# Optimization experiments

Measured on AMD Instinct MI355X. Metric: run time of the kernel, lower is better.

## Reference

```python
import jax, jax.numpy as jnp
import numpy as np

B, C1, C2 = 8, 256, 256
Cc = 128          # c = int(c2 * e)
RED = 16          # reduction in FrequencyModulation
HEADS = 8
HD = Cc // HEADS  # 16
HH, WW = 32, 32


def _c1x1(x, w, b=None):
    # 1x1 conv as channel contraction; w: [out_c, in_c]
    y = jnp.einsum('bchw,oc->bohw', x, w)
    return y if b is None else y + b[None, :, None, None]


def setup_inputs() -> dict:
    key = jax.random.key(0)
    ks = jax.random.split(key, 22)
    s = 0.02
    p = {}
    p['x'] = jax.random.normal(ks[0], (B, C1, HH, WW), jnp.float32)
    p['cv1_w'] = jax.random.normal(ks[1], (2 * Cc, C1), jnp.float32) * s
    p['cv1_b'] = jnp.zeros((2 * Cc,), jnp.float32)
    # FrequencyModulation params
    p['fm_w1'] = jax.random.normal(ks[2], (Cc // RED, Cc), jnp.float32) * s
    p['fm_w2'] = jax.random.normal(ks[3], (Cc, Cc // RED), jnp.float32) * s
    p['ca_w1'] = jax.random.normal(ks[4], (Cc // RED, Cc), jnp.float32) * s
    p['ca_w2'] = jax.random.normal(ks[5], (Cc, Cc // RED), jnp.float32) * s
    # TokenStatisticsSelfAttention params (qkv_bias=False)
    p['qkv_w'] = jax.random.normal(ks[6], (3 * Cc, Cc), jnp.float32) * s
    p['tproj_w'] = jax.random.normal(ks[7], (Cc, Cc), jnp.float32) * s
    p['tproj_b'] = jnp.zeros((Cc,), jnp.float32)
    # SpatialQuantizedRouter params
    p['dw_w'] = jax.random.normal(ks[8], (Cc, 1, 3, 3), jnp.float32) * s  # depthwise
    p['dw_b'] = jnp.zeros((Cc,), jnp.float32)
    p['rt_w'] = jax.random.normal(ks[9], (1, Cc), jnp.float32) * s
    p['rt_b'] = jnp.zeros((1,), jnp.float32)
    p['q_w'] = jax.random.normal(ks[10], (Cc, Cc), jnp.float32) * s
    p['k_w'] = jax.random.normal(ks[11], (Cc, Cc), jnp.float32) * s
    p['v_w'] = jax.random.normal(ks[12], (Cc, Cc), jnp.float32) * s
    p['sproj_w'] = jax.random.normal(ks[13], (Cc, Cc), jnp.float32) * s
    p['sproj_b'] = jnp.zeros((Cc,), jnp.float32)
    p['cv2_w'] = jax.random.normal(ks[14], (C2, 3 * Cc), jnp.float32) * s
    p['cv2_b'] = jnp.zeros((C2,), jnp.float32)
    return p


def _forward(x, cv1_w, cv1_b, fm_w1, fm_w2, ca_w1, ca_w2, qkv_w, tproj_w,
             tproj_b, dw_w, dw_b, rt_w, rt_b, q_w, k_w, v_w, sproj_w,
             sproj_b, cv2_w, cv2_b):
    Bb, _, H, W = x.shape
    N = H * W
    y = _c1x1(x, cv1_w, cv1_b)
    y0, y1 = y[:, :Cc], y[:, Cc:]

    # ---- Branch 1: FrequencyModulation ----
    xf = jnp.fft.rfft2(y1.astype(jnp.float32), norm='ortho')  # [B,c,H,W//2+1] complex
    mag = jnp.abs(xf)
    pooled = mag.mean(axis=(-2, -1))                          # [B,c]
    fw = jax.nn.sigmoid(jax.nn.relu(pooled @ fm_w1.T) @ fm_w2.T)  # [B,c]
    # mag*fw*exp(i*phase) == fw * xf  (fw is real, per batch/channel)
    xs = jnp.fft.irfft2(xf * fw[:, :, None, None].astype(jnp.complex64),
                        s=(H, W), norm='ortho')               # [B,c,H,W]
    ca = jax.nn.sigmoid(jax.nn.relu(xs.mean(axis=(-2, -1)) @ ca_w1.T) @ ca_w2.T)
    freq_out = xs * ca[:, :, None, None]

    # ---- Branch 2: TokenStatisticsSelfAttention ----
    xt = y1.reshape(Bb, Cc, N).transpose(0, 2, 1)             # [B,N,c]
    qkv = (xt @ qkv_w.T).reshape(Bb, N, 3, HEADS, HD).transpose(2, 0, 3, 1, 4)
    q, k, v = qkv[0], qkv[1], qkv[2]                          # [B,h,N,d]
    var_v = jnp.var(v, axis=-1, ddof=1, keepdims=True)        # [B,h,N,1] (unbiased)
    var_k = jnp.var(k, axis=-1, ddof=1, keepdims=True)
    attn = jax.nn.softmax(jnp.einsum('bhnx,bhmx->bhnm', var_v, var_k) * (HD ** -0.5), axis=-1)
    to = jnp.einsum('bhnm,bhmd->bhnd', attn, v).transpose(0, 2, 1, 3).reshape(Bb, N, Cc)
    stat_out = ((to @ tproj_w.T) + tproj_b).transpose(0, 2, 1).reshape(Bb, Cc, H, W)

    # ---- Branch 3: SpatialQuantizedRouter (training-mode blend) ----
    x_local = jax.lax.conv_general_dilated(
        y1, dw_w, (1, 1), 'SAME', feature_group_count=Cc,
        dimension_numbers=('NCHW', 'OIHW', 'NCHW')) + dw_b[None, :, None, None]
    p_route = jax.nn.sigmoid(y1.mean(axis=(-2, -1)) @ rt_w.T + rt_b)  # [B,1]
    qb = jnp.sign(_c1x1(y1, q_w).reshape(Bb, Cc, N))
    kb = jnp.sign(_c1x1(y1, k_w).reshape(Bb, Cc, N))
    vv = _c1x1(y1, v_w).reshape(Bb, Cc, N)
    a2 = jax.nn.softmax(jnp.einsum('bcn,bcm->bnm', qb, kb) * (Cc ** -0.5), axis=-1)
    # torch: bmm(v, attn.T) -> out[b,c,n] = sum_m v[b,c,m]*attn[b,n,m]
    ob = jnp.einsum('bcm,bnm->bcn', vv, a2).reshape(Bb, Cc, H, W)
    out_bin = _c1x1(ob, sproj_w, sproj_b)
    alpha = p_route.reshape(Bb, 1, 1, 1)
    spat_out = (1.0 - alpha) * x_local + alpha * out_bin

    attn_out = freq_out + stat_out + spat_out
    yc = jnp.concatenate([y0, y1, attn_out], axis=1)          # [B,3c,H,W]
    out = _c1x1(yc, cv2_w, cv2_b)
    return x + out  # add: shortcut and c1 == c2


def reference(x, cv1_w, cv1_b, fm_w1, fm_w2, ca_w1, ca_w2, qkv_w, tproj_w,
              tproj_b, dw_w, dw_b, rt_w, rt_b, q_w, k_w, v_w, sproj_w,
              sproj_b, cv2_w, cv2_b):
    return _forward(x, cv1_w, cv1_b, fm_w1, fm_w2, ca_w1, ca_w2, qkv_w,
                    tproj_w, tproj_b, dw_w, dw_b, rt_w, rt_b, q_w, k_w, v_w,
                    sproj_w, sproj_b, cv2_w, cv2_b)
```

## Files before the change

### kernel.cpp

```cpp
#include <hip/hip_runtime.h>
#include <math.h>

#define BATCH 8
#define NPIX 1024

typedef __attribute__((ext_vector_type(8))) short short8v;
typedef __attribute__((ext_vector_type(4))) float f32x4;

__device__ inline unsigned short f2bf(float x) {
  unsigned int u = __float_as_uint(x);
  return (unsigned short)((u + 0x7FFFu + ((u >> 16) & 1u)) >> 16);
}
__device__ inline float bf2f(unsigned short h) {
  return __uint_as_float((unsigned int)h << 16);
}
__device__ inline unsigned long long pack4bf(float a, float b, float c, float d) {
  return (unsigned long long)(unsigned short)f2bf(a) |
         ((unsigned long long)(unsigned short)f2bf(b) << 16) |
         ((unsigned long long)(unsigned short)f2bf(c) << 32) |
         ((unsigned long long)(unsigned short)f2bf(d) << 48);
}

__global__ __launch_bounds__(256) void convw_kernel(
    const float* __restrict__ cv1_w, const float* __restrict__ qkv_w,
    const float* __restrict__ tproj_w, const float* __restrict__ sproj_w,
    const float* __restrict__ cv2_w, const float* __restrict__ q_w,
    const float* __restrict__ k_w, const float* __restrict__ v_w,
    short* __restrict__ wb) {
  int i = blockIdx.x * 256 + threadIdx.x;
  float v;
  if (i < 65536) v = cv1_w[i];
  else if (i < 163840) {
    int j = i - 65536;
    if (j < 49152) v = qkv_w[j];
    else {
      int jj = j - 49152, wsel = jj >> 14, r = jj & 16383;
      v = (wsel == 0) ? q_w[r] : (wsel == 1) ? k_w[r] : v_w[r];
    }
  }
  else if (i < 180224) v = tproj_w[i - 163840];
  else if (i < 196608) v = sproj_w[i - 180224];
  else v = cv2_w[i - 196608];
  wb[i] = (short)f2bf(v);
}

template<int MODE, bool HAS_BIAS, bool HAS_RES, bool XF32T, bool EMIT_HI>
__global__ __launch_bounds__(256) void mgemm_kernel(
    const short* __restrict__ Wb, const void* __restrict__ Xsrc, int ldx,
    const float* __restrict__ bias, const float* __restrict__ res,
    void* __restrict__ Y0, void* __restrict__ Y1,
    int K, long sXT, long sY, long sR, int tStride, int tOff) {
  __shared__ __align__(16) short As[64][40];
  __shared__ __align__(16) short Bs[64][40];
  const int b = blockIdx.z;
  const int n0 = blockIdx.x * 64, m0 = blockIdx.y * 64;
  const int tid = threadIdx.x;
  const int l = tid & 63, w = tid >> 6;
  const int wm = w >> 1, wn = w & 1;
  const int sr = tid >> 2, sko = (tid & 3) * 8;
  const int xr = tid >> 3, xcg = (tid & 7) * 8;
  const int fr = l & 15, fk = (l >> 4) * 8;
  f32x4 acc[2][2] = {};
  for (int k0 = 0; k0 < K; k0 += 32) {
    *(uint4*)&As[sr][sko] = *(const uint4*)(Wb + (long)(m0 + sr) * K + k0 + sko);
    if (XF32T) {
      const float* Xf = (const float*)Xsrc + (long)b * sXT;
      const float4 xa = *(const float4*)(Xf + (long)(k0 + xr) * 1024 + n0 + xcg);
      const float4 xb = *(const float4*)(Xf + (long)(k0 + xr) * 1024 + n0 + xcg + 4);
      Bs[xcg + 0][xr] = (short)f2bf(xa.x); Bs[xcg + 1][xr] = (short)f2bf(xa.y);
      Bs[xcg + 2][xr] = (short)f2bf(xa.z); Bs[xcg + 3][xr] = (short)f2bf(xa.w);
      Bs[xcg + 4][xr] = (short)f2bf(xb.x); Bs[xcg + 5][xr] = (short)f2bf(xb.y);
      Bs[xcg + 6][xr] = (short)f2bf(xb.z); Bs[xcg + 7][xr] = (short)f2bf(xb.w);
    } else {
      const short* Xb = (const short*)Xsrc + (long)b * sXT;
      *(uint4*)&Bs[sr][sko] = *(const uint4*)(Xb + (long)(n0 + sr) * ldx + k0 + sko);
    }
    __syncthreads();
    short8v a0 = *(short8v*)&As[wm * 32 + fr][fk];
    short8v a1 = *(short8v*)&As[wm * 32 + 16 + fr][fk];
    short8v b0 = *(short8v*)&Bs[wn * 32 + fr][fk];
    short8v b1 = *(short8v*)&Bs[wn * 32 + 16 + fr][fk];
    acc[0][0] = __builtin_amdgcn_mfma_f32_16x16x32_bf16(a0, b0, acc[0][0], 0, 0, 0);
    acc[0][1] = __builtin_amdgcn_mfma_f32_16x16x32_bf16(a0, b1, acc[0][1], 0, 0, 0);
    acc[1][0] = __builtin_amdgcn_mfma_f32_16x16x32_bf16(a1, b0, acc[1][0], 0, 0, 0);
    acc[1][1] = __builtin_amdgcn_mfma_f32_16x16x32_bf16(a1, b1, acc[1][1], 0, 0, 0);
    __syncthreads();
  }
#pragma unroll
  for (int tm = 0; tm < 2; tm++) {
    const int m_base = m0 + wm * 32 + tm * 16 + (l >> 4) * 4;
#pragma unroll
    for (int tn = 0; tn < 2; tn++) {
      const int n = n0 + wn * 32 + tn * 16 + (l & 15);
      float v0 = acc[tm][tn][0], v1 = acc[tm][tn][1];
      float v2 = acc[tm][tn][2], v3 = acc[tm][tn][3];
      if (HAS_BIAS) {
        v0 += bias[m_base]; v1 += bias[m_base + 1];
        v2 += bias[m_base + 2]; v3 += bias[m_base + 3];
      }
      if (HAS_RES) {
        v0 += res[(long)b * sR + (long)(m_base + 0) * 1024 + n];
        v1 += res[(long)b * sR + (long)(m_base + 1) * 1024 + n];
        v2 += res[(long)b * sR + (long)(m_base + 2) * 1024 + n];
        v3 += res[(long)b * sR + (long)(m_base + 3) * 1024 + n];
      }
      if (MODE == 0) {
        float* Y = (float*)Y0 + (long)b * sY + n;
        Y[(long)(m_base + 0) * 1024] = v0; Y[(long)(m_base + 1) * 1024] = v1;
        Y[(long)(m_base + 2) * 1024] = v2; Y[(long)(m_base + 3) * 1024] = v3;
      } else if (MODE == 1) {
        short* Y = (short*)Y0 + (long)b * sY + n;
        Y[(long)(m_base + 0) * 1024] = (short)f2bf(v0);
        Y[(long)(m_base + 1) * 1024] = (short)f2bf(v1);
        Y[(long)(m_base + 2) * 1024] = (short)f2bf(v2);
        Y[(long)(m_base + 3) * 1024] = (short)f2bf(v3);
      } else if (MODE == 2) {
        *(unsigned long long*)((short*)Y0 + ((long)b * 1024 + n) * tStride +
                               tOff + m_base) = pack4bf(v0, v1, v2, v3);
        if (EMIT_HI && m_base >= 128) {
          float* Y = (float*)Y1 + ((long)b * 128 + m_base - 128) * 1024 + n;
          Y[0] = v0; Y[1024] = v1; Y[2048] = v2; Y[3072] = v3;
        }
      } else {
        if (m0 < 384) {
          float* Y = (float*)Y0 + (long)b * 384 * 1024 + (long)m_base * 1024 + n;
          Y[0] = v0; Y[1024] = v1; Y[2048] = v2; Y[3072] = v3;
        } else {
          *(unsigned long long*)((short*)Y1 + ((long)b * 1024 + n) * 384 +
                                 (m_base - 384)) = pack4bf(v0, v1, v2, v3);
        }
      }
    }
  }
}

__global__ __launch_bounds__(256) void fftpool_kernel(
    const float* __restrict__ y1, float* __restrict__ pooled, float* __restrict__ m1) {
  const int bc = blockIdx.x;
  const float* img = y1 + (long)bc * NPIX;
  __shared__ float im[1024];
  __shared__ float Gr[32][17], Gi[32][17];
  __shared__ float cs[32], sn[32];
  __shared__ float red[256];
  const int t = threadIdx.x;
  if (t < 32) {
    float ang = -0.19634954084936207f * (float)t;
    __sincosf(ang, &sn[t], &cs[t]);
  }
  float lsum = 0.f;
  for (int i = t; i < 1024; i += 256) { float v = img[i]; im[i] = v; lsum += v; }
  red[t] = lsum;
  __syncthreads();
  for (int s = 128; s > 0; s >>= 1) {
    if (t < s) red[t] += red[t + s];
    __syncthreads();
  }
  if (t == 0) m1[bc] = red[0] * (1.f / 1024.f);
  for (int i = t; i < 544; i += 256) {
    int h = i / 17, v = i % 17;
    float ar = 0.f, ai = 0.f;
    for (int w2 = 0; w2 < 32; w2++) {
      int k = (v * w2) & 31;
      float x = im[h * 32 + w2];
      ar += x * cs[k]; ai += x * sn[k];
    }
    Gr[h][v] = ar; Gi[h][v] = ai;
  }
  __syncthreads();
  float asum = 0.f;
  for (int i = t; i < 544; i += 256) {
    int u = i / 17, v = i % 17;
    float xr = 0.f, xi = 0.f;
    for (int h = 0; h < 32; h++) {
      int k = (u * h) & 31;
      float gr = Gr[h][v], gi = Gi[h][v];
      xr += gr * cs[k] - gi * sn[k];
      xi += gr * sn[k] + gi * cs[k];
    }
    asum += sqrtf(xr * xr + xi * xi);
  }
  red[t] = asum;
  __syncthreads();
  for (int s = 128; s > 0; s >>= 1) {
    if (t < s) red[t] += red[t + s];
    __syncthreads();
  }
  if (t == 0) pooled[bc] = red[0] * (1.f / (32.f * 544.f));
}

__global__ __launch_bounds__(128) void gates_kernel(
    const float* __restrict__ pooled, const float* __restrict__ m1,
    const float* __restrict__ fm_w1, const float* __restrict__ fm_w2,
    const float* __restrict__ ca_w1, const float* __restrict__ ca_w2,
    const float* __restrict__ rt_w, const float* __restrict__ rt_b,
    float* __restrict__ g, float* __restrict__ alpha, float* __restrict__ maxvk) {
  const int b = blockIdx.x, t = threadIdx.x;
  __shared__ float h1[8], fwv[128], xsm[128], h2[8];
  if (t < 8) maxvk[b * 8 + t] = 0.f;
  const float* pb = pooled + b * 128;
  const float* mb = m1 + b * 128;
  if (t < 8) {
    float s = 0.f;
    for (int c = 0; c < 128; c++) s += pb[c] * fm_w1[t * 128 + c];
    h1[t] = fmaxf(s, 0.f);
  }
  __syncthreads();
  {
    float s = 0.f;
    for (int r = 0; r < 8; r++) s += h1[r] * fm_w2[t * 8 + r];
    float fw = 1.f / (1.f + __expf(-s));
    fwv[t] = fw; xsm[t] = fw * mb[t];
  }
  __syncthreads();
  if (t < 8) {
    float s = 0.f;
    for (int c = 0; c < 128; c++) s += xsm[c] * ca_w1[t * 128 + c];
    h2[t] = fmaxf(s, 0.f);
  }
  __syncthreads();
  {
    float s = 0.f;
    for (int r = 0; r < 8; r++) s += h2[r] * ca_w2[t * 8 + r];
    float ca = 1.f / (1.f + __expf(-s));
    g[b * 128 + t] = fwv[t] * ca;
  }
  if (t == 0) {
    float s = 0.f;
    for (int c = 0; c < 128; c++) s += mb[c] * rt_w[c];
    s += rt_b[0];
    alpha[b] = 1.f / (1.f + __expf(-s));
  }
}

__global__ __launch_bounds__(256) void varmax_kernel(
    const float* __restrict__ qkvb, float* __restrict__ var_k,
    float* __restrict__ var_v, float* __restrict__ maxvk,
    short* __restrict__ vTb) {
  const int bh = blockIdx.x;
  const int chunk = blockIdx.y;
  const int b = bh >> 3, h = bh & 7;
  __shared__ float red[256];
  __shared__ float trans[16][256];
  const int n = chunk * 256 + threadIdx.x;
  const float* kb = qkvb + ((long)b * 384 + 128 + h * 16) * NPIX;
  const float* vb = qkvb + ((long)b * 384 + 256 + h * 16) * NPIX;
  float xk[16], xv[16], sk = 0.f, sv = 0.f;
#pragma unroll
  for (int d = 0; d < 16; d++) {
    xk[d] = kb[(long)d * NPIX + n]; sk += xk[d];
    xv[d] = vb[(long)d * NPIX + n]; sv += xv[d];
  }
  float mk = sk * (1.f / 16.f), mv = sv * (1.f / 16.f);
  float vk_ = 0.f, vv_ = 0.f;
#pragma unroll
  for (int d = 0; d < 16; d++) {
    float a = xk[d] - mk; vk_ += a * a;
    float c = xv[d] - mv; vv_ += c * c;
  }
  vk_ *= (1.f / 15.f); vv_ *= (1.f / 15.f);
  var_k[(long)bh * NPIX + n] = vk_;
  var_v[(long)bh * NPIX + n] = vv_;
#pragma unroll
  for (int d = 0; d < 16; d++) trans[d][threadIdx.x] = xv[d];
  __syncthreads();
  {
    int d = threadIdx.x >> 4, mc = threadIdx.x & 15;
    __align__(16) short tmp[16];
#pragma unroll
    for (int e = 0; e < 16; e++) tmp[e] = (short)f2bf(trans[d][mc * 16 + e]);
    short* dst = vTb + ((long)bh * 16 + d) * 1024 + chunk * 256 + mc * 16;
    *(uint4*)dst = *(uint4*)tmp;
    *(uint4*)(dst + 8) = *(uint4*)(tmp + 8);
  }
  red[threadIdx.x] = vk_;
  __syncthreads();
  for (int s = 128; s > 0; s >>= 1) {
    if (threadIdx.x < s) red[threadIdx.x] = fmaxf(red[threadIdx.x], red[threadIdx.x + s]);
    __syncthreads();
  }
  if (threadIdx.x == 0)
    atomicMax((int*)(maxvk + bh), __float_as_int(red[0]));
}

__global__ __launch_bounds__(256) void stat_mfma_kernel(
    const short* __restrict__ vTb, const float* __restrict__ var_k,
    const float* __restrict__ var_v, const float* __restrict__ maxvk,
    short* __restrict__ tcT) {
  const int bh = blockIdx.x;
  const int b = bh >> 3, h = bh & 7;
  const int n0 = blockIdx.y * 64;
  const int tid = threadIdx.x;
  const int l = tid & 63, w = tid >> 6;
  const int ln = l & 15, lk = l >> 4;
  const int n = n0 + w * 16 + ln;
  __shared__ float vk[1024];
  for (int i = tid; i < 1024; i += 256) vk[i] = var_k[(long)bh * 1024 + i];
  const float cn = var_v[(long)bh * 1024 + n] * 0.25f;
  const float mv = maxvk[bh];
  const short* arow = vTb + ((long)bh * 16 + ln) * 1024 + lk * 8;
  __syncthreads();
  f32x4 acc = {};
  float psum = 0.f;
  for (int m0 = 0; m0 < 1024; m0 += 32) {
    short8v afrag = *(const short8v*)(arow + m0);
    short8v bfrag;
#pragma unroll
    for (int j = 0; j < 8; j++) {
      float wv = __expf(cn * (vk[m0 + lk * 8 + j] - mv));
      psum += wv;
      bfrag[j] = (short)f2bf(wv);
    }
    acc = __builtin_amdgcn_mfma_f32_16x16x32_bf16(afrag, bfrag, acc, 0, 0, 0);
  }
  psum += __shfl_xor(psum, 16);
  psum += __shfl_xor(psum, 32);
  const float inv = 1.f / psum;
  *(unsigned long long*)(tcT + ((long)b * 1024 + n) * 128 + h * 16 + lk * 4) =
      pack4bf(acc[0] * inv, acc[1] * inv, acc[2] * inv, acc[3] * inv);
}

__global__ __launch_bounds__(256) void pack_kernel(
    const short* __restrict__ sqkvT,
    unsigned long long* __restrict__ qbits, unsigned long long* __restrict__ kbits) {
  const int wave = threadIdx.x >> 6, lane = threadIdx.x & 63;
  const long p = (long)blockIdx.x * 4 + wave;
  const short* base = sqkvT + p * 384;
  unsigned long long q0 = __ballot(bf2f((unsigned short)base[lane]) > 0.f);
  unsigned long long q1 = __ballot(bf2f((unsigned short)base[64 + lane]) > 0.f);
  unsigned long long k0 = __ballot(bf2f((unsigned short)base[128 + lane]) > 0.f);
  unsigned long long k1 = __ballot(bf2f((unsigned short)base[192 + lane]) > 0.f);
  if (lane == 0) {
    qbits[p * 2] = q0; qbits[p * 2 + 1] = q1;
    kbits[p * 2] = k0; kbits[p * 2 + 1] = k1;
  }
}

__global__ __launch_bounds__(256) void obgemm_kernel(
    const short* __restrict__ pvb, const unsigned long long* __restrict__ qbits,
    const unsigned long long* __restrict__ kbits, short* __restrict__ pnum,
    float* __restrict__ pden) {
  const int b = blockIdx.z;
  const int sp = blockIdx.y;
  const int n0 = blockIdx.x * 64;
  const int kb0 = sp * 256;
  __shared__ __align__(16) short As[128][40];
  __shared__ __align__(16) unsigned long long kbsh[256][2];
  const int tid = threadIdx.x;
  const int l = tid & 63, w = tid >> 6;
  const int ln = l & 15, lk = l >> 4;
  const int n = n0 + w * 16 + ln;
  const unsigned long long q0 = qbits[((long)b * 1024 + n) * 2];
  const unsigned long long q1 = qbits[((long)b * 1024 + n) * 2 + 1];
  *(uint4*)&kbsh[tid][0] = *(const uint4*)(kbits + ((long)b * 1024 + kb0 + tid) * 2);
  const float fs = 0.08838834764831845f;
  const int sc = tid >> 1, sh = (tid & 1) * 16;
  const short* pvrow = pvb + ((long)b * 128 + sc) * 1024 + kb0;
  f32x4 acc[8] = {};
  float psum = 0.f;
  for (int ks = 0; ks < 8; ks++) {
    *(uint4*)&As[sc][sh] = *(const uint4*)(pvrow + ks * 32 + sh);
    *(uint4*)&As[sc][sh + 8] = *(const uint4*)(pvrow + ks * 32 + sh + 8);
    __syncthreads();
    const int mloc = ks * 32 + lk * 8;
    short8v bfrag;
#pragma unroll
    for (int j = 0; j < 8; j++) {
      unsigned long long kw0 = kbsh[mloc + j][0];
      unsigned long long kw1 = kbsh[mloc + j][1];
      int ham = __popcll(kw0 ^ q0) + __popcll(kw1 ^ q1);
      float wv = __expf((float)(128 - 2 * ham) * fs);
      psum += wv;
      bfrag[j] = (short)f2bf(wv);
    }
#pragma unroll
    for (int ct = 0; ct < 8; ct++) {
      short8v afrag = *(short8v*)&As[ct * 16 + ln][lk * 8];
      acc[ct] = __builtin_amdgcn_mfma_f32_16x16x32_bf16(afrag, bfrag, acc[ct], 0, 0, 0);
    }
    __syncthreads();
  }
  short* dst = pnum + (((long)sp * 8 + b) * 128) * 1024 + n;
#pragma unroll
  for (int ct = 0; ct < 8; ct++)
#pragma unroll
    for (int i = 0; i < 4; i++)
      dst[(long)(ct * 16 + lk * 4 + i) * 1024] = (short)f2bf(acc[ct][i]);
  psum += __shfl_xor(psum, 16);
  psum += __shfl_xor(psum, 32);
  if (lk == 0)
    pden[((long)sp * 8 + b) * 1024 + n] = psum;
}

__global__ __launch_bounds__(256) void dwcombine_kernel(
    const float* __restrict__ y1, float* __restrict__ attn,
    const float* __restrict__ dw_w, const float* __restrict__ dw_b,
    const short* __restrict__ pnum, const float* __restrict__ pden,
    const float* __restrict__ sproj_b, const float* __restrict__ g,
    const float* __restrict__ alpha) {
  const int bc = blockIdx.x;
  const int b = bc >> 7, cx = bc & 127;
  const float* img = y1 + (long)bc * NPIX;
  float* dst = attn + (long)bc * NPIX;
  float w[9];
#pragma unroll
  for (int i = 0; i < 9; i++) w[i] = dw_w[cx * 9 + i];
  const float bias = dw_b[cx];
  const float a = alpha[b];
  const float gg = g[bc];
  const float sb = sproj_b[cx];
  const long ns = 8L * 128 * 1024;
  const long ds = 8L * 1024;
  const long nbase = (long)bc * 1024;
  const long dbase = (long)b * 1024;
  for (int i = threadIdx.x; i < 1024; i += 256) {
    int h = i >> 5, wx = i & 31;
    float s = bias;
#pragma unroll
    for (int ky = 0; ky < 3; ky++) {
      int hh = h + ky - 1;
      if (hh < 0 || hh > 31) continue;
#pragma unroll
      for (int kx = 0; kx < 3; kx++) {
        int ww2 = wx + kx - 1;
        if (ww2 < 0 || ww2 > 31) continue;
        s += img[hh * 32 + ww2] * w[ky * 3 + kx];
      }
    }
    float num = bf2f((unsigned short)pnum[nbase + i]) +
                bf2f((unsigned short)pnum[nbase + i + ns]) +
                bf2f((unsigned short)pnum[nbase + i + 2 * ns]) +
                bf2f((unsigned short)pnum[nbase + i + 3 * ns]);
    float den = pden[dbase + i] + pden[dbase + i + ds] +
                pden[dbase + i + 2 * ds] + pden[dbase + i + 3 * ds];
    float obv = num / den + sb;
    dst[i] = gg * img[i] + (1.f - a) * s + a * obv;
  }
}

extern "C" void kernel_launch(void* const* d_in, const int* in_sizes, int n_in,
                              void* d_out, int out_size, void* d_ws, size_t ws_size,
                              hipStream_t stream) {
  const float* x = (const float*)d_in[0];
  const float* cv1_w = (const float*)d_in[1];
  const float* cv1_b = (const float*)d_in[2];
  const float* fm_w1 = (const float*)d_in[3];
  const float* fm_w2 = (const float*)d_in[4];
  const float* ca_w1 = (const float*)d_in[5];
  const float* ca_w2 = (const float*)d_in[6];
  const float* qkv_w = (const float*)d_in[7];
  const float* tproj_w = (const float*)d_in[8];
  const float* tproj_b = (const float*)d_in[9];
  const float* dw_w = (const float*)d_in[10];
  const float* dw_b = (const float*)d_in[11];
  const float* rt_w = (const float*)d_in[12];
  const float* rt_b = (const float*)d_in[13];
  const float* q_w = (const float*)d_in[14];
  const float* k_w = (const float*)d_in[15];
  const float* v_w = (const float*)d_in[16];
  const float* sproj_w = (const float*)d_in[17];
  const float* sproj_b = (const float*)d_in[18];
  const float* cv2_w = (const float*)d_in[19];
  const float* cv2_b = (const float*)d_in[20];
  float* out = (float*)d_out;

  char* wsp = (char*)d_ws;
  size_t off = 0;
  auto alloc = [&](size_t bytes) {
    void* p = wsp + off;
    off += (bytes + 255) & ~(size_t)255;
    return p;
  };
  float* qkvb = (float*)alloc(8UL * 384 * 1024 * 4);
  float* y1 = (float*)alloc(8UL * 128 * 1024 * 4);
  float* attn = (float*)alloc(8UL * 128 * 1024 * 4);
  short* ycT = (short*)alloc(8UL * 1024 * 384 * 2);
  short* sqkvT = (short*)alloc(8UL * 1024 * 384 * 2);
  short* tcT = (short*)alloc(8UL * 1024 * 128 * 2);
  short* pvb = (short*)alloc(8UL * 128 * 1024 * 2);
  short* wb = (short*)alloc(294912UL * 2);
  short* vTb = (short*)alloc(64UL * 16 * 1024 * 2);
  float* pden = (float*)alloc(4UL * 8 * 1024 * 4);
  float* var_k = (float*)alloc(8UL * 8 * 1024 * 4);
  float* var_v = (float*)alloc(8UL * 8 * 1024 * 4);
  float* maxvk = (float*)alloc(64 * 4);
  float* pooled = (float*)alloc(1024 * 4);
  float* m1 = (float*)alloc(1024 * 4);
  float* g = (float*)alloc(1024 * 4);
  float* alpha = (float*)alloc(8 * 4);
  unsigned long long* qbits = (unsigned long long*)alloc(8192UL * 2 * 8);
  unsigned long long* kbits = (unsigned long long*)alloc(8192UL * 2 * 8);
  short* pnum = (short*)qkvb;
  const short* cv1b = wb;
  const short* qsb = wb + 65536;
  const short* tprojb = wb + 163840;
  const short* sprojb = wb + 180224;
  const short* cv2b = wb + 196608;
  if (off > ws_size) return;

  dim3 blk(256);
  convw_kernel<<<dim3(1152), blk, 0, stream>>>(cv1_w, qkv_w, tproj_w, sproj_w,
                                               cv2_w, q_w, k_w, v_w, wb);
  mgemm_kernel<2, true, false, true, true><<<dim3(16, 4, 8), blk, 0, stream>>>(
      cv1b, x, 0, cv1_b, nullptr, ycT, y1, 256, 256L * 1024, 0, 0, 384, 0);
  fftpool_kernel<<<dim3(1024), blk, 0, stream>>>(y1, pooled, m1);
  gates_kernel<<<dim3(8), dim3(128), 0, stream>>>(pooled, m1, fm_w1, fm_w2,
                                                  ca_w1, ca_w2, rt_w, rt_b, g,
                                                  alpha, maxvk);
  mgemm_kernel<3, false, false, false, false><<<dim3(16, 12, 8), blk, 0, stream>>>(
      qsb, ycT + 128, 384, nullptr, nullptr, qkvb, sqkvT, 128, 1024L * 384,
      0, 0, 0, 0);
  varmax_kernel<<<dim3(64, 4), blk, 0, stream>>>(qkvb, var_k, var_v, maxvk, vTb);
  stat_mfma_kernel<<<dim3(64, 16), blk, 0, stream>>>(vTb, var_k, var_v, maxvk, tcT);
  pack_kernel<<<dim3(2048), blk, 0, stream>>>(sqkvT, qbits, kbits);
  mgemm_kernel<1, false, false, false, false><<<dim3(16, 2, 8), blk, 0, stream>>>(
      sprojb, sqkvT + 256, 384, nullptr, nullptr, pvb, nullptr, 128,
      1024L * 384, 128L * 1024, 0, 0, 0);
  obgemm_kernel<<<dim3(16, 4, 8), blk, 0, stream>>>(pvb, qbits, kbits, pnum, pden);
  dwcombine_kernel<<<dim3(1024), blk, 0, stream>>>(y1, attn, dw_w, dw_b, pnum,
                                                   pden, sproj_b, g, alpha);
  mgemm_kernel<2, true, true, false, false><<<dim3(16, 2, 8), blk, 0, stream>>>(
      tprojb, tcT, 128, tproj_b, attn, ycT, nullptr, 128, 1024L * 128, 0,
      128L * 1024, 384, 256);
  mgemm_kernel<0, true, true, false, false><<<dim3(16, 4, 8), blk, 0, stream>>>(
      cv2b, ycT, 384, cv2_b, x, out, nullptr, 384, 1024L * 384, 256L * 1024,
      256L * 1024, 0, 0);
}
```

Baseline: 120.8 us.

## Fuse gates into fftpool via last-block atomic and merge pack into pv GEMM

Removes the separate gates kernel by having the last fftpool block for each batch, detected with an atomic counter, compute the gating MLP and routing alpha. Zeroing of maxvk and the counters moves into the weight-conversion kernel. The sign-bit pack kernel is folded into a new dedicated 64x64 MFMA GEMM kernel that computes pvb and then ballots q/k signs. Together these cut two kernel launches, at the cost of atomics, threadfences and a serialized tail inside fftpool.

```diff
diff --git a/kernel.cpp b/kernel.cpp
--- a/kernel.cpp
+++ b/kernel.cpp
@@ -26,7 +26,11 @@
     const float* __restrict__ tproj_w, const float* __restrict__ sproj_w,
     const float* __restrict__ cv2_w, const float* __restrict__ q_w,
     const float* __restrict__ k_w, const float* __restrict__ v_w,
-    short* __restrict__ wb) {
+    short* __restrict__ wb, float* __restrict__ maxvk, int* __restrict__ fcnt) {
+  if (blockIdx.x == 0) {
+    if (threadIdx.x < 64) maxvk[threadIdx.x] = 0.f;
+    else if (threadIdx.x < 72) fcnt[threadIdx.x - 64] = 0;
+  }
   int i = blockIdx.x * 256 + threadIdx.x;
   float v;
   if (i < 65536) v = cv1_w[i];
@@ -134,14 +138,79 @@
   }
 }
 
+__global__ __launch_bounds__(256) void pvpack_kernel(
+    const short* __restrict__ Wb, const short* __restrict__ sqkvT,
+    short* __restrict__ pvb,
+    unsigned long long* __restrict__ qbits, unsigned long long* __restrict__ kbits) {
+  __shared__ __align__(16) short As[64][40];
+  __shared__ __align__(16) short Bs[64][40];
+  const int b = blockIdx.z;
+  const int n0 = blockIdx.x * 64, m0 = blockIdx.y * 64;
+  const int tid = threadIdx.x;
+  const int l = tid & 63, w = tid >> 6;
+  const int wm = w >> 1, wn = w & 1;
+  const int sr = tid >> 2, sko = (tid & 3) * 8;
+  const int fr = l & 15, fk = (l >> 4) * 8;
+  const short* Xb = sqkvT + 256 + (long)b * 1024 * 384;
+  f32x4 acc[2][2] = {};
+  for (int k0 = 0; k0 < 128; k0 += 32) {
+    *(uint4*)&As[sr][sko] = *(const uint4*)(Wb + (long)(m0 + sr) * 128 + k0 + sko);
+    *(uint4*)&Bs[sr][sko] = *(const uint4*)(Xb + (long)(n0 + sr) * 384 + k0 + sko);
+    __syncthreads();
+    short8v a0 = *(short8v*)&As[wm * 32 + fr][fk];
+    short8v a1 = *(short8v*)&As[wm * 32 + 16 + fr][fk];
+    short8v b0 = *(short8v*)&Bs[wn * 32 + fr][fk];
+    short8v b1 = *(short8v*)&Bs[wn * 32 + 16 + fr][fk];
+    acc[0][0] = __builtin_amdgcn_mfma_f32_16x16x32_bf16(a0, b0, acc[0][0], 0, 0, 0);
+    acc[0][1] = __builtin_amdgcn_mfma_f32_16x16x32_bf16(a0, b1, acc[0][1], 0, 0, 0);
+    acc[1][0] = __builtin_amdgcn_mfma_f32_16x16x32_bf16(a1, b0, acc[1][0], 0, 0, 0);
+    acc[1][1] = __builtin_amdgcn_mfma_f32_16x16x32_bf16(a1, b1, acc[1][1], 0, 0, 0);
+    __syncthreads();
+  }
+#pragma unroll
+  for (int tm = 0; tm < 2; tm++) {
+    const int m_base = m0 + wm * 32 + tm * 16 + (l >> 4) * 4;
+#pragma unroll
+    for (int tn = 0; tn < 2; tn++) {
+      const int n = n0 + wn * 32 + tn * 16 + (l & 15);
+      short* Y = pvb + (long)b * 128 * 1024 + n;
+      Y[(long)(m_base + 0) * 1024] = (short)f2bf(acc[tm][tn][0]);
+      Y[(long)(m_base + 1) * 1024] = (short)f2bf(acc[tm][tn][1]);
+      Y[(long)(m_base + 2) * 1024] = (short)f2bf(acc[tm][tn][2]);
+      Y[(long)(m_base + 3) * 1024] = (short)f2bf(acc[tm][tn][3]);
+    }
+  }
+  const int wgid = blockIdx.x + 16 * (blockIdx.y + 2 * blockIdx.z);
+  const long wbase = ((long)wgid * 4 + w) * 8;
+#pragma unroll
+  for (int j = 0; j < 8; j++) {
+    const long p = wbase + j;
+    const short* base = sqkvT + p * 384;
+    unsigned long long q0 = __ballot(bf2f((unsigned short)base[l]) > 0.f);
+    unsigned long long q1 = __ballot(bf2f((unsigned short)base[64 + l]) > 0.f);
+    unsigned long long k0 = __ballot(bf2f((unsigned short)base[128 + l]) > 0.f);
+    unsigned long long k1 = __ballot(bf2f((unsigned short)base[192 + l]) > 0.f);
+    if (l == 0) {
+      qbits[p * 2] = q0; qbits[p * 2 + 1] = q1;
+      kbits[p * 2] = k0; kbits[p * 2 + 1] = k1;
+    }
+  }
+}
+
 __global__ __launch_bounds__(256) void fftpool_kernel(
-    const float* __restrict__ y1, float* __restrict__ pooled, float* __restrict__ m1) {
+    const float* __restrict__ y1, float* __restrict__ pooled, float* __restrict__ m1,
+    const float* __restrict__ fm_w1, const float* __restrict__ fm_w2,
+    const float* __restrict__ ca_w1, const float* __restrict__ ca_w2,
+    const float* __restrict__ rt_w, const float* __restrict__ rt_b,
+    float* __restrict__ g, float* __restrict__ alpha, int* __restrict__ fcnt) {
   const int bc = blockIdx.x;
+  const int b = bc >> 7;
   const float* img = y1 + (long)bc * NPIX;
   __shared__ float im[1024];
   __shared__ float Gr[32][17], Gi[32][17];
   __shared__ float cs[32], sn[32];
   __shared__ float red[256];
+  __shared__ int lastFlag;
   const int t = threadIdx.x;
   if (t < 32) {
     float ang = -0.19634954084936207f * (float)t;
@@ -186,49 +255,51 @@
     __syncthreads();
   }
   if (t == 0) pooled[bc] = red[0] * (1.f / (32.f * 544.f));
-}
-
-__global__ __launch_bounds__(128) void gates_kernel(
-    const float* __restrict__ pooled, const float* __restrict__ m1,
-    const float* __restrict__ fm_w1, const float* __restrict__ fm_w2,
-    const float* __restrict__ ca_w1, const float* __restrict__ ca_w2,
-    const float* __restrict__ rt_w, const float* __restrict__ rt_b,
-    float* __restrict__ g, float* __restrict__ alpha, float* __restrict__ maxvk) {
-  const int b = blockIdx.x, t = threadIdx.x;
-  __shared__ float h1[8], fwv[128], xsm[128], h2[8];
-  if (t < 8) maxvk[b * 8 + t] = 0.f;
-  const float* pb = pooled + b * 128;
-  const float* mb = m1 + b * 128;
-  if (t < 8) {
-    float s = 0.f;
-    for (int c = 0; c < 128; c++) s += pb[c] * fm_w1[t * 128 + c];
-    h1[t] = fmaxf(s, 0.f);
-  }
-  __syncthreads();
-  {
-    float s = 0.f;
-    for (int r = 0; r < 8; r++) s += h1[r] * fm_w2[t * 8 + r];
-    float fw = 1.f / (1.f + __expf(-s));
-    fwv[t] = fw; xsm[t] = fw * mb[t];
-  }
-  __syncthreads();
-  if (t < 8) {
-    float s = 0.f;
-    for (int c = 0; c < 128; c++) s += xsm[c] * ca_w1[t * 128 + c];
-    h2[t] = fmaxf(s, 0.f);
-  }
-  __syncthreads();
-  {
-    float s = 0.f;
-    for (int r = 0; r < 8; r++) s += h2[r] * ca_w2[t * 8 + r];
-    float ca = 1.f / (1.f + __expf(-s));
-    g[b * 128 + t] = fwv[t] * ca;
-  }
   if (t == 0) {
-    float s = 0.f;
-    for (int c = 0; c < 128; c++) s += mb[c] * rt_w[c];
-    s += rt_b[0];
-    alpha[b] = 1.f / (1.f + __expf(-s));
+    __threadfence();
+    int prev = atomicAdd(&fcnt[b], 1);
+    lastFlag = (prev == 127) ? 1 : 0;
+  }
+  __syncthreads();
+  if (lastFlag) {
+    __threadfence();
+    float* h1 = im;
+    float* fwv = im + 8;
+    float* xsm = im + 140;
+    float* h2 = im + 272;
+    const float* pb = pooled + b * 128;
+    const float* mb = m1 + b * 128;
+    if (t < 8) {
+      float s = 0.f;
+      for (int c = 0; c < 128; c++) s += pb[c] * fm_w1[t * 128 + c];
+      h1[t] = fmaxf(s, 0.f);
+    }
+    __syncthreads();
+    if (t < 128) {
+      float s = 0.f;
+      for (int r = 0; r < 8; r++) s += h1[r] * fm_w2[t * 8 + r];
+      float fw = 1.f / (1.f + __expf(-s));
+      fwv[t] = fw; xsm[t] = fw * mb[t];
+    }
+    __syncthreads();
+    if (t < 8) {
+      float s = 0.f;
+      for (int c = 0; c < 128; c++) s += xsm[c] * ca_w1[t * 128 + c];
+      h2[t] = fmaxf(s, 0.f);
+    }
+    __syncthreads();
+    if (t < 128) {
+      float s = 0.f;
+      for (int r = 0; r < 8; r++) s += h2[r] * ca_w2[t * 8 + r];
+      float ca = 1.f / (1.f + __expf(-s));
+      g[b * 128 + t] = fwv[t] * ca;
+    }
+    if (t == 0) {
+      float s = 0.f;
+      for (int c = 0; c < 128; c++) s += mb[c] * rt_w[c];
+      s += rt_b[0];
+      alpha[b] = 1.f / (1.f + __expf(-s));
+    }
   }
 }
 
@@ -317,22 +388,6 @@
   const float inv = 1.f / psum;
   *(unsigned long long*)(tcT + ((long)b * 1024 + n) * 128 + h * 16 + lk * 4) =
       pack4bf(acc[0] * inv, acc[1] * inv, acc[2] * inv, acc[3] * inv);
-}
-
-__global__ __launch_bounds__(256) void pack_kernel(
-    const short* __restrict__ sqkvT,
-    unsigned long long* __restrict__ qbits, unsigned long long* __restrict__ kbits) {
-  const int wave = threadIdx.x >> 6, lane = threadIdx.x & 63;
-  const long p = (long)blockIdx.x * 4 + wave;
-  const short* base = sqkvT + p * 384;
-  unsigned long long q0 = __ballot(bf2f((unsigned short)base[lane]) > 0.f);
-  unsigned long long q1 = __ballot(bf2f((unsigned short)base[64 + lane]) > 0.f);
-  unsigned long long k0 = __ballot(bf2f((unsigned short)base[128 + lane]) > 0.f);
-  unsigned long long k1 = __ballot(bf2f((unsigned short)base[192 + lane]) > 0.f);
-  if (lane == 0) {
-    qbits[p * 2] = q0; qbits[p * 2 + 1] = q1;
-    kbits[p * 2] = k0; kbits[p * 2 + 1] = k1;
-  }
 }
 
 __global__ __launch_bounds__(256) void obgemm_kernel(
@@ -487,6 +542,7 @@
   float* m1 = (float*)alloc(1024 * 4);
   float* g = (float*)alloc(1024 * 4);
   float* alpha = (float*)alloc(8 * 4);
+  int* fcnt = (int*)alloc(8 * 4);
   unsigned long long* qbits = (unsigned long long*)alloc(8192UL * 2 * 8);
   unsigned long long* kbits = (unsigned long long*)alloc(8192UL * 2 * 8);
   short* pnum = (short*)qkvb;
@@ -499,22 +555,20 @@
 
   dim3 blk(256);
   convw_kernel<<<dim3(1152), blk, 0, stream>>>(cv1_w, qkv_w, tproj_w, sproj_w,
-                                               cv2_w, q_w, k_w, v_w, wb);
+                                               cv2_w, q_w, k_w, v_w, wb, maxvk,
+                                               fcnt);
   mgemm_kernel<2, true, false, true, true><<<dim3(16, 4, 8), blk, 0, stream>>>(
       cv1b, x, 0, cv1_b, nullptr, ycT, y1, 256, 256L * 1024, 0, 0, 384, 0);
-  fftpool_kernel<<<dim3(1024), blk, 0, stream>>>(y1, pooled, m1);
-  gates_kernel<<<dim3(8), dim3(128), 0, stream>>>(pooled, m1, fm_w1, fm_w2,
-                                                  ca_w1, ca_w2, rt_w, rt_b, g,
-                                                  alpha, maxvk);
+  fftpool_kernel<<<dim3(1024), blk, 0, stream>>>(y1, pooled, m1, fm_w1, fm_w2,
+                                                 ca_w1, ca_w2, rt_w, rt_b, g,
+                                                 alpha, fcnt);
   mgemm_kernel<3, false, false, false, false><<<dim3(16, 12, 8), blk, 0, stream>>>(
       qsb, ycT + 128, 384, nullptr, nullptr, qkvb, sqkvT, 128, 1024L * 384,
       0, 0, 0, 0);
   varmax_kernel<<<dim3(64, 4), blk, 0, stream>>>(qkvb, var_k, var_v, maxvk, vTb);
   stat_mfma_kernel<<<dim3(64, 16), blk, 0, stream>>>(vTb, var_k, var_v, maxvk, tcT);
-  pack_kernel<<<dim3(2048), blk, 0, stream>>>(sqkvT, qbits, kbits);
-  mgemm_kernel<1, false, false, false, false><<<dim3(16, 2, 8), blk, 0, stream>>>(
-      sprojb, sqkvT + 256, 384, nullptr, nullptr, pvb, nullptr, 128,
-      1024L * 384, 128L * 1024, 0, 0, 0);
+  pvpack_kernel<<<dim3(16, 2, 8), blk, 0, stream>>>(sprojb, sqkvT, pvb, qbits,
+                                                    kbits);
   obgemm_kernel<<<dim3(16, 4, 8), blk, 0, stream>>>(pvb, qbits, kbits, pnum, pden);
   dwcombine_kernel<<<dim3(1024), blk, 0, stream>>>(y1, attn, dw_w, dw_b, pnum,
                                                    pden, sproj_b, g, alpha);
```

Measured after the change: 137.6 us. 13.9% more time.
